# Kernel optimization log

Hardware: AMD Instinct MI355X
Metric: run time of the kernel (lower is better)

The kernel has to match this reference:

```python
import jax, jax.numpy as jnp
import numpy as np

H, NB, D = 16, 64, 1024
HID = 64  # gate MLP hidden width


def setup_inputs() -> dict:
    key = jax.random.key(0)
    ks = jax.random.split(key, 10)
    B, T = 4, 2048
    delta = jax.random.normal(ks[0], (B, T, H, NB), dtype=jnp.float32)
    content_emb = jax.random.normal(ks[1], (B, T, D), dtype=jnp.float32)
    omega = jax.random.normal(ks[2], (H, NB), dtype=jnp.float32)
    # learned parameters
    log_Q = jnp.zeros((H, NB), dtype=jnp.float32)
    log_R = jnp.zeros((H, NB), dtype=jnp.float32)
    log_sigma0 = jnp.full((H, NB), -2.0, dtype=jnp.float32)
    W1 = jax.random.normal(ks[3], (D, HID), dtype=jnp.float32) / np.sqrt(D)
    b1 = jnp.zeros((HID,), dtype=jnp.float32)
    W2 = jax.random.normal(ks[4], (HID, H * NB), dtype=jnp.float32) / np.sqrt(HID)
    b2 = jnp.zeros((H * NB,), dtype=jnp.float32)
    return {"delta": delta, "content_emb": content_emb, "omega": omega,
            "log_Q": log_Q, "log_R": log_R, "log_sigma0": log_sigma0,
            "W1": W1, "b1": b1, "W2": W2, "b2": b2}


def reference(delta, content_emb, omega, log_Q, log_R, log_sigma0, W1, b1, W2, b2):
    B, T, _, _ = delta.shape
    Q = jnp.exp(log_Q)            # (H, NB)
    R = jnp.exp(log_R)            # (H, NB)
    sigma0 = jnp.exp(log_sigma0)  # (H, NB)

    theta_sq = (delta * omega) ** 2  # (B, T, H, NB)

    # landmark gate MLP (exact GELU, as torch default)
    h = jax.nn.gelu(content_emb @ W1 + b1, approximate=False)  # (B, T, HID)
    gates = jax.nn.sigmoid(h @ W2 + b2).reshape(B, T, H, NB)

    def step(sigma, xs):
        theta_sq_t, gate_t = xs  # (B, H, NB) each
        sigma = sigma + Q * theta_sq_t
        K = sigma / (sigma + R)
        sigma = sigma * (1.0 - gate_t * K)
        return sigma, sigma

    init = jnp.broadcast_to(sigma0, (B, H, NB))
    xs = (jnp.swapaxes(theta_sq, 0, 1), jnp.swapaxes(gates, 0, 1))  # (T, B, H, NB)
    _, sigma_seq = jax.lax.scan(step, init, xs)
    sigma = jnp.swapaxes(sigma_seq, 0, 1)  # (B, T, H, NB)
    return sigma, gates
```

## Files before the change

kernel.cpp:

```cpp
#include <hip/hip_runtime.h>
#include <math.h>

#define H_   16
#define NB_  64
#define D_   1024
#define HID_ 64
#define B_   4
#define T_   2048
#define ROWS (B_*T_)
#define HNB  (H_*NB_)

typedef short v8s __attribute__((ext_vector_type(8)));
typedef float v4f __attribute__((ext_vector_type(4)));

__device__ __forceinline__ float gelu_exact(float x) {
    return 0.5f * x * (1.0f + erff(x * 0.7071067811865476f));
}
__device__ __forceinline__ float sigmoidf(float x) {
    return 1.0f / (1.0f + expf(-x));
}
__device__ __forceinline__ ushort f2bf(float x) {
    union { float f; unsigned u; } v; v.f = x;
    unsigned r = v.u + 0x7fffu + ((v.u >> 16) & 1u);
    return (ushort)(r >> 16);
}

__global__ __launch_bounds__(256) void k_prep(const float* __restrict__ W1,
                                              const float* __restrict__ W2,
                                              ushort* __restrict__ w1t,
                                              ushort* __restrict__ w2t) {
    __shared__ float ls[64][65];
    const int t   = threadIdx.x;
    const int blk = blockIdx.x;
    if (blk < 16) {
        const int k0 = blk * 64;
        #pragma unroll
        for (int q = 0; q < 4; ++q) {
            int idx = q * 256 + t;
            int r = idx >> 4, c4 = idx & 15;
            *(float4*)&ls[r][c4 * 4] =
                *(const float4*)&W1[(size_t)(k0 + r) * 64 + c4 * 4];
        }
        __syncthreads();
        const int col = t >> 2, kq = t & 3;
        ushort out[16];
        #pragma unroll
        for (int e = 0; e < 16; ++e) out[e] = f2bf(ls[kq * 16 + e][col]);
        *(uint4*)&w1t[(size_t)col * 1024 + k0 + kq * 16]     = *(uint4*)&out[0];
        *(uint4*)&w1t[(size_t)col * 1024 + k0 + kq * 16 + 8] = *(uint4*)&out[8];
    } else {
        const int n0 = (blk - 16) * 64;
        #pragma unroll
        for (int q = 0; q < 4; ++q) {
            int idx = q * 256 + t;
            int r = idx >> 4, c4 = idx & 15;
            *(float4*)&ls[r][c4 * 4] =
                *(const float4*)&W2[(size_t)r * HNB + n0 + c4 * 4];
        }
        __syncthreads();
        const int n = t >> 2, kq = t & 3;
        ushort out[16];
        #pragma unroll
        for (int e = 0; e < 16; ++e) out[e] = f2bf(ls[kq * 16 + e][n]);
        *(uint4*)&w2t[(size_t)(n0 + n) * 64 + kq * 16]     = *(uint4*)&out[0];
        *(uint4*)&w2t[(size_t)(n0 + n) * 64 + kq * 16 + 8] = *(uint4*)&out[8];
    }
}

__global__ __launch_bounds__(256) void k_gemm1_mfma(const float* __restrict__ X,
                                                    const ushort* __restrict__ w1t,
                                                    const float* __restrict__ b1,
                                                    ushort* __restrict__ hbuf) {
    __shared__ ushort Al[32 * 128];
    __shared__ ushort Bl[64 * 128];
    const int t    = threadIdx.x;
    const int r0   = blockIdx.x * 32;
    const int w    = t >> 6;
    const int lane = t & 63;
    const int lo   = lane & 15;
    const int hi   = lane >> 4;
    const int mt   = w & 1;
    const int nh   = w >> 1;
    const int arow = t >> 3, aseg = t & 7;
    const int brow = t >> 2, bseg = t & 3;

    v4f acc0 = {0.f,0.f,0.f,0.f}, acc1 = {0.f,0.f,0.f,0.f};

    for (int c = 0; c < 8; ++c) {
        float xv[16];
        const float* xp = &X[(size_t)(r0 + arow) * D_ + c * 128 + aseg * 16];
        #pragma unroll
        for (int i = 0; i < 4; ++i) *(float4*)&xv[i*4] = *(const float4*)&xp[i*4];
        ushort wv[32];
        const ushort* wp = &w1t[(size_t)brow * 1024 + c * 128 + bseg * 32];
        #pragma unroll
        for (int i = 0; i < 4; ++i) *(uint4*)&wv[i*8] = *(const uint4*)&wp[i*8];

        __syncthreads();
        #pragma unroll
        for (int j8 = 0; j8 < 2; ++j8) {
            const int k = aseg * 16 + j8 * 8;
            union { ushort u[8]; v8s v; } pa;
            #pragma unroll
            for (int e = 0; e < 8; ++e) pa.u[e] = f2bf(xv[j8 * 8 + e]);
            *(v8s*)&Al[arow * 128 + (k ^ ((arow & 7) << 3))] = pa.v;
        }
        #pragma unroll
        for (int j8 = 0; j8 < 4; ++j8) {
            const int k = bseg * 32 + j8 * 8;
            *(v8s*)&Bl[brow * 128 + (k ^ ((brow & 7) << 3))] = *(v8s*)&wv[j8 * 8];
        }
        __syncthreads();

        const int rowa = mt * 16 + lo;
        #pragma unroll
        for (int kk = 0; kk < 4; ++kk) {
            const int k   = kk * 32 + hi * 8;
            const int sw  = k ^ ((lo & 7) << 3);
            v8s af  = *(v8s*)&Al[rowa * 128 + sw];
            v8s b0  = *(v8s*)&Bl[(nh * 32 + lo) * 128 + sw];
            v8s b1v = *(v8s*)&Bl[(nh * 32 + 16 + lo) * 128 + sw];
            acc0 = __builtin_amdgcn_mfma_f32_16x16x32_bf16(af, b0,  acc0, 0, 0, 0);
            acc1 = __builtin_amdgcn_mfma_f32_16x16x32_bf16(af, b1v, acc1, 0, 0, 0);
        }
    }
    #pragma unroll
    for (int nt = 0; nt < 2; ++nt) {
        v4f a = nt ? acc1 : acc0;
        const int col = nh * 32 + nt * 16 + lo;
        const float bb = b1[col];
        #pragma unroll
        for (int j = 0; j < 4; ++j) {
            const int row = r0 + mt * 16 + hi * 4 + j;
            hbuf[(size_t)row * HID_ + col] = f2bf(gelu_exact(a[j] + bb));
        }
    }
}

__global__ __launch_bounds__(256) void k_gemm2_mfma(const ushort* __restrict__ hbuf,
                                                    const ushort* __restrict__ w2t,
                                                    const float* __restrict__ b2,
                                                    float* __restrict__ gates) {
    __shared__ ushort Ah[64 * 64];
    __shared__ ushort Bh[256 * 64];
    const int t    = threadIdx.x;
    const int r0   = (blockIdx.x >> 2) * 64;
    const int n0   = (blockIdx.x & 3) * 256;
    const int w    = t >> 6;
    const int lane = t & 63;
    const int lo   = lane & 15;
    const int hi   = lane >> 4;

    {
        const int row = t >> 2, seg = t & 3;
        uint4 v0 = *(const uint4*)&hbuf[(size_t)(r0 + row) * 64 + seg * 16];
        uint4 v1 = *(const uint4*)&hbuf[(size_t)(r0 + row) * 64 + seg * 16 + 8];
        const int sw = (row & 7) << 3;
        *(uint4*)&Ah[row * 64 + ((seg * 16) ^ sw)]     = v0;
        *(uint4*)&Ah[row * 64 + ((seg * 16 + 8) ^ sw)] = v1;
    }
    #pragma unroll
    for (int q = 0; q < 4; ++q) {
        const int pi  = q * 256 + t;
        const int n   = pi >> 2, seg = pi & 3;
        uint4 v0 = *(const uint4*)&w2t[(size_t)(n0 + n) * 64 + seg * 16];
        uint4 v1 = *(const uint4*)&w2t[(size_t)(n0 + n) * 64 + seg * 16 + 8];
        const int sw = (n & 7) << 3;
        *(uint4*)&Bh[n * 64 + ((seg * 16) ^ sw)]     = v0;
        *(uint4*)&Bh[n * 64 + ((seg * 16 + 8) ^ sw)] = v1;
    }
    __syncthreads();

    v4f acc[4][4];
    #pragma unroll
    for (int mt = 0; mt < 4; ++mt)
        #pragma unroll
        for (int nt = 0; nt < 4; ++nt) acc[mt][nt] = (v4f){0.f,0.f,0.f,0.f};

    #pragma unroll
    for (int kc = 0; kc < 2; ++kc) {
        const int k  = kc * 32 + hi * 8;
        const int sw = k ^ ((lo & 7) << 3);
        v8s af[4];
        #pragma unroll
        for (int mt = 0; mt < 4; ++mt)
            af[mt] = *(v8s*)&Ah[(mt * 16 + lo) * 64 + sw];
        #pragma unroll
        for (int nt = 0; nt < 4; ++nt) {
            v8s bf = *(v8s*)&Bh[(w * 64 + nt * 16 + lo) * 64 + sw];
            #pragma unroll
            for (int mt = 0; mt < 4; ++mt)
                acc[mt][nt] = __builtin_amdgcn_mfma_f32_16x16x32_bf16(af[mt], bf, acc[mt][nt], 0, 0, 0);
        }
    }

    #pragma unroll
    for (int nt = 0; nt < 4; ++nt) {
        const int col = n0 + w * 64 + nt * 16 + lo;
        const float bb = b2[col];
        #pragma unroll
        for (int mt = 0; mt < 4; ++mt) {
            #pragma unroll
            for (int j = 0; j < 4; ++j) {
                const int row = r0 + mt * 16 + hi * 4 + j;
                gates[(size_t)row * HNB + col] = sigmoidf(acc[mt][nt][j] + bb);
            }
        }
    }
}

#define TT_    32
#define SEGK   8
#define SEGLEN (T_/SEGK)
#define WARMT  3

#define LD8(A, G, grp) { \
    _Pragma("unroll") \
    for (int u = 0; u < 8; ++u) { \
        A[u] = pa[((grp)*8 + u) * 128]; \
        G[u] = pa[((grp)*8 + u) * 128 + 64]; \
    } }

#define CP8(A, G, grp) { \
    _Pragma("unroll") \
    for (int u = 0; u < 8; ++u) { \
        float a   = A[u]; \
        float omg = G[u]; \
        float aR  = a + R; \
        float pc  = fmaf(omg, a, R); \
        float den = sigma + aR; \
        float s   = sigma + a; \
        float pp  = fmaf(omg, sigma, pc); \
        float rc  = __builtin_amdgcn_rcpf(den); \
        float tt  = s * pp; \
        sigma     = tt * rc; \
        ps[((grp)*8 + u) * 64] = sigma; \
    } }

__global__ __launch_bounds__(256) void k_scan_seg(
        const float* __restrict__ delta,
        const float* __restrict__ gates,
        const float* __restrict__ omega,
        const float* __restrict__ log_Q,
        const float* __restrict__ log_R,
        const float* __restrict__ log_s0,
        float* __restrict__ sig) {
    __shared__ float tg_lds[2][TT_][2][64];
    __shared__ float sg_lds[2][TT_][64];
    const int tid = threadIdx.x;
    const int blk = blockIdx.x;
    const int bh  = blk >> 3;
    const int seg = blk & 7;
    const int b   = bh >> 4;
    const int h   = bh & 15;
    const size_t base = (size_t)b * T_ * HNB + h * NB_;
    const int wv   = tid >> 6;
    const int lane = tid & 63;

    const int warm   = (seg == 0) ? 0 : WARMT;
    const int ntiles = SEGLEN / TT_ + warm;
    const int tstart = seg * SEGLEN - warm * TT_;

    float R = 0.f, sigma = 0.f;
    float sc0=0,sc1=0,sc2=0,sc3=0;
    const int col4 = lane & 15;
    const int rg   = lane >> 4;
    const float* dp = delta + base + col4 * 4;
    const float* gp = gates + base + col4 * 4;

    if (wv == 0) {
        const int hn = h * NB_ + lane;
        R     = expf(log_R[hn]);
        sigma = expf(log_s0[hn]);
    } else if (wv == 1) {
        const int hn4 = h * NB_ + col4 * 4;
        float4 om4 = *(const float4*)&omega[hn4];
        float4 lq4 = *(const float4*)&log_Q[hn4];
        sc0 = expf(lq4.x) * om4.x * om4.x;
        sc1 = expf(lq4.y) * om4.y * om4.y;
        sc2 = expf(lq4.z) * om4.z * om4.z;
        sc3 = expf(lq4.w) * om4.w * om4.w;
    }

    for (int p = 0; p <= ntiles + 1; ++p) {
        if (wv == 0) {
            if (p >= 1 && p <= ntiles) {
                const int buf = (p - 1) & 1;
                const float* pa = &tg_lds[buf][0][0][lane];
                float*       ps = &sg_lds[buf][0][lane];
                float a0[8], g0[8], a1[8], g1[8];
                LD8(a0, g0, 0);
                LD8(a1, g1, 1);
                CP8(a0, g0, 0); LD8(a0, g0, 2);
                CP8(a1, g1, 1); LD8(a1, g1, 3);
                CP8(a0, g0, 2);
                CP8(a1, g1, 3);
            }
        } else if (wv == 1) {
            if (p < ntiles) {
                const int buf = p & 1;
                const int t0  = tstart + p * TT_;
                #pragma unroll
                for (int it = 0; it < 8; ++it) {
                    const int row = it * 4 + rg;
                    float4 d = *(const float4*)&dp[(size_t)(t0 + row) * HNB];
                    float4 a;
                    a.x = (sc0 * d.x) * d.x;
                    a.y = (sc1 * d.y) * d.y;
                    a.z = (sc2 * d.z) * d.z;
                    a.w = (sc3 * d.w) * d.w;
                    *(float4*)&tg_lds[buf][row][0][col4 * 4] = a;
                }
            }
        } else if (wv == 2) {
            if (p < ntiles) {
                const int buf = p & 1;
                const int t0  = tstart + p * TT_;
                #pragma unroll
                for (int it = 0; it < 8; ++it) {
                    const int row = it * 4 + rg;
                    float4 g = *(const float4*)&gp[(size_t)(t0 + row) * HNB];
                    float4 o;
                    o.x = 1.0f - g.x; o.y = 1.0f - g.y;
                    o.z = 1.0f - g.z; o.w = 1.0f - g.w;
                    *(float4*)&tg_lds[buf][row][1][col4 * 4] = o;
                }
            }
        } else {
            const int tile = p - 2;
            if (tile >= warm && tile < ntiles) {
                const int buf = p & 1;
                const int t0  = tstart + tile * TT_;
                float* op = sig + base + col4 * 4;
                #pragma unroll
                for (int it = 0; it < 8; ++it) {
                    const int row = it * 4 + rg;
                    float4 v = *(const float4*)&sg_lds[buf][row][col4 * 4];
                    *(float4*)&op[(size_t)(t0 + row) * HNB] = v;
                }
            }
        }
        __syncthreads();
    }
}

extern "C" void kernel_launch(void* const* d_in, const int* in_sizes, int n_in,
                              void* d_out, int out_size, void* d_ws, size_t ws_size,
                              hipStream_t stream) {
    const float* delta   = (const float*)d_in[0];
    const float* content = (const float*)d_in[1];
    const float* omega   = (const float*)d_in[2];
    const float* log_Q   = (const float*)d_in[3];
    const float* log_R   = (const float*)d_in[4];
    const float* log_s0  = (const float*)d_in[5];
    const float* W1      = (const float*)d_in[6];
    const float* b1      = (const float*)d_in[7];
    const float* W2      = (const float*)d_in[8];
    const float* b2      = (const float*)d_in[9];

    float* sig_out   = (float*)d_out;
    float* gates_out = sig_out + (size_t)ROWS * HNB;

    const size_t n_h   = (size_t)ROWS * HID_;
    const size_t n_w1t = (size_t)HID_ * D_;
    const size_t n_w2t = (size_t)HNB * HID_;
    const size_t need  = (n_h + n_w1t + n_w2t) * sizeof(ushort);

    ushort *hbuf, *w1t, *w2t;
    if (ws_size >= need) {
        hbuf = (ushort*)d_ws;
    } else {
        hbuf = (ushort*)sig_out;
    }
    w1t = hbuf + n_h;
    w2t = w1t + n_w1t;

    k_prep<<<32, 256, 0, stream>>>(W1, W2, w1t, w2t);
    k_gemm1_mfma<<<ROWS / 32, 256, 0, stream>>>(content, w1t, b1, hbuf);
    k_gemm2_mfma<<<(ROWS / 64) * 4, 256, 0, stream>>>(hbuf, w2t, b2, gates_out);
    k_scan_seg<<<B_ * H_ * SEGK, 256, 0, stream>>>(delta, gates_out, omega,
                                                   log_Q, log_R, log_s0, sig_out);
}
```

Baseline: 57.42 us.

## Fuse gate GEMM2 and sigmoid into the segmented scan kernel

```diff
diff --git a/kernel.cpp b/kernel.cpp
--- a/kernel.cpp
+++ b/kernel.cpp
@@ -236,6 +236,163 @@
         sigma     = tt * rc; \
         ps[((grp)*8 + u) * 64] = sigma; \
     } }
+
+__global__ __launch_bounds__(256) void k_scan_fused(
+        const float* __restrict__ delta,
+        const ushort* __restrict__ hbuf,
+        const ushort* __restrict__ w2t,
+        const float* __restrict__ b2,
+        const float* __restrict__ omega,
+        const float* __restrict__ log_Q,
+        const float* __restrict__ log_R,
+        const float* __restrict__ log_s0,
+        float* __restrict__ gates,
+        float* __restrict__ sig) {
+    __shared__ float  tg_lds[2][TT_][2][64];
+    __shared__ float  sg_lds[2][TT_][64];
+    __shared__ ushort w2s[64 * 64];
+    const int tid = threadIdx.x;
+    const int blk = blockIdx.x;
+    const int bh  = blk >> 3;
+    const int seg = blk & 7;
+    const int b   = bh >> 4;
+    const int h   = bh & 15;
+    const size_t base = (size_t)b * T_ * HNB + h * NB_;
+    const int wv   = tid >> 6;
+    const int lane = tid & 63;
+    const int lo   = lane & 15;
+    const int hi   = lane >> 4;
+
+    const int warm   = (seg == 0) ? 0 : WARMT;
+    const int ntiles = SEGLEN / TT_ + warm;
+    const int tstart = seg * SEGLEN - warm * TT_;
+
+    float R = 0.f, sigma = 0.f;
+    float sc0=0,sc1=0,sc2=0,sc3=0;
+    float bb0=0,bb1=0,bb2=0,bb3=0;
+    const int col4 = lane & 15;
+    const int rg   = lane >> 4;
+    const float* dp = delta + base + col4 * 4;
+
+    if (wv == 0) {
+        const int hn = h * NB_ + lane;
+        R     = expf(log_R[hn]);
+        sigma = expf(log_s0[hn]);
+    } else if (wv == 1) {
+        const int hn4 = h * NB_ + col4 * 4;
+        float4 om4 = *(const float4*)&omega[hn4];
+        float4 lq4 = *(const float4*)&log_Q[hn4];
+        sc0 = expf(lq4.x) * om4.x * om4.x;
+        sc1 = expf(lq4.y) * om4.y * om4.y;
+        sc2 = expf(lq4.z) * om4.z * om4.z;
+        sc3 = expf(lq4.w) * om4.w * om4.w;
+    } else if (wv == 2) {
+        const ushort* wp = &w2t[(size_t)(h * 64 + lane) * 64];
+        const int sw = (lane & 7) << 3;
+        #pragma unroll
+        for (int s4 = 0; s4 < 4; ++s4) {
+            uint4 v0 = *(const uint4*)&wp[s4 * 16];
+            uint4 v1 = *(const uint4*)&wp[s4 * 16 + 8];
+            *(uint4*)&w2s[lane * 64 + ((s4 * 16) ^ sw)]     = v0;
+            *(uint4*)&w2s[lane * 64 + ((s4 * 16 + 8) ^ sw)] = v1;
+        }
+        bb0 = b2[h * 64 +  0 + lo];
+        bb1 = b2[h * 64 + 16 + lo];
+        bb2 = b2[h * 64 + 32 + lo];
+        bb3 = b2[h * 64 + 48 + lo];
+    }
+
+    for (int p = 0; p <= ntiles + 1; ++p) {
+        if (wv == 0) {
+            if (p >= 1 && p <= ntiles) {
+                const int buf = (p - 1) & 1;
+                const float* pa = &tg_lds[buf][0][0][lane];
+                float*       ps = &sg_lds[buf][0][lane];
+                float a0[8], g0[8], a1[8], g1[8];
+                LD8(a0, g0, 0);
+                LD8(a1, g1, 1);
+                CP8(a0, g0, 0); LD8(a0, g0, 2);
+                CP8(a1, g1, 1); LD8(a1, g1, 3);
+                CP8(a0, g0, 2);
+                CP8(a1, g1, 3);
+            }
+        } else if (wv == 1) {
+            if (p < ntiles) {
+                const int buf = p & 1;
+                const int t0  = tstart + p * TT_;
+                #pragma unroll
+                for (int it = 0; it < 8; ++it) {
+                    const int row = it * 4 + rg;
+                    float4 d = *(const float4*)&dp[(size_t)(t0 + row) * HNB];
+                    float4 a;
+                    a.x = (sc0 * d.x) * d.x;
+                    a.y = (sc1 * d.y) * d.y;
+                    a.z = (sc2 * d.z) * d.z;
+                    a.w = (sc3 * d.w) * d.w;
+                    *(float4*)&tg_lds[buf][row][0][col4 * 4] = a;
+                }
+            }
+        } else if (wv == 2) {
+            if (p < ntiles) {
+                const int buf = p & 1;
+                const int t0  = tstart + p * TT_;
+                const size_t grow = (size_t)b * T_ + t0;
+                v4f acc[2][4];
+                #pragma unroll
+                for (int mt = 0; mt < 2; ++mt)
+                    #pragma unroll
+                    for (int nt = 0; nt < 4; ++nt) acc[mt][nt] = (v4f){0.f,0.f,0.f,0.f};
+                #pragma unroll
+                for (int ks = 0; ks < 2; ++ks) {
+                    const int k  = ks * 32 + hi * 8;
+                    const int sw = k ^ ((lo & 7) << 3);
+                    v8s af[2];
+                    #pragma unroll
+                    for (int mt = 0; mt < 2; ++mt)
+                        af[mt] = *(const v8s*)&hbuf[(grow + mt * 16 + lo) * HID_ + k];
+                    #pragma unroll
+                    for (int nt = 0; nt < 4; ++nt) {
+                        v8s bf = *(v8s*)&w2s[(nt * 16 + lo) * 64 + sw];
+                        #pragma unroll
+                        for (int mt = 0; mt < 2; ++mt)
+                            acc[mt][nt] = __builtin_amdgcn_mfma_f32_16x16x32_bf16(af[mt], bf, acc[mt][nt], 0, 0, 0);
+                    }
+                }
+                const bool wout = (p >= warm);
+                #pragma unroll
+                for (int nt = 0; nt < 4; ++nt) {
+                    const float bb = (nt == 0) ? bb0 : (nt == 1) ? bb1 : (nt == 2) ? bb2 : bb3;
+                    const int col = nt * 16 + lo;
+                    #pragma unroll
+                    for (int mt = 0; mt < 2; ++mt) {
+                        #pragma unroll
+                        for (int j = 0; j < 4; ++j) {
+                            const int row = mt * 16 + hi * 4 + j;
+                            float g = sigmoidf(acc[mt][nt][j] + bb);
+                            tg_lds[buf][row][1][col] = 1.0f - g;
+                            if (wout)
+                                gates[(grow + row) * HNB + h * NB_ + col] = g;
+                        }
+                    }
+                }
+            }
+        } else {
+            const int tile = p - 2;
+            if (tile >= warm && tile < ntiles) {
+                const int buf = p & 1;
+                const int t0  = tstart + tile * TT_;
+                float* op = sig + base + col4 * 4;
+                #pragma unroll
+                for (int it = 0; it < 8; ++it) {
+                    const int row = it * 4 + rg;
+                    float4 v = *(const float4*)&sg_lds[buf][row][col4 * 4];
+                    *(float4*)&op[(size_t)(t0 + row) * HNB] = v;
+                }
+            }
+        }
+        __syncthreads();
+    }
+}
 
 __global__ __launch_bounds__(256) void k_scan_seg(
         const float* __restrict__ delta,
@@ -366,18 +523,23 @@
     const size_t n_w2t = (size_t)HNB * HID_;
     const size_t need  = (n_h + n_w1t + n_w2t) * sizeof(ushort);
 
-    ushort *hbuf, *w1t, *w2t;
     if (ws_size >= need) {
-        hbuf = (ushort*)d_ws;
+        ushort* hbuf = (ushort*)d_ws;
+        ushort* w1t  = hbuf + n_h;
+        ushort* w2t  = w1t + n_w1t;
+        k_prep<<<32, 256, 0, stream>>>(W1, W2, w1t, w2t);
+        k_gemm1_mfma<<<ROWS / 32, 256, 0, stream>>>(content, w1t, b1, hbuf);
+        k_scan_fused<<<B_ * H_ * SEGK, 256, 0, stream>>>(delta, hbuf, w2t, b2,
+                                                         omega, log_Q, log_R,
+                                                         log_s0, gates_out, sig_out);
     } else {
-        hbuf = (ushort*)sig_out;
-    }
-    w1t = hbuf + n_h;
-    w2t = w1t + n_w1t;
-
-    k_prep<<<32, 256, 0, stream>>>(W1, W2, w1t, w2t);
-    k_gemm1_mfma<<<ROWS / 32, 256, 0, stream>>>(content, w1t, b1, hbuf);
-    k_gemm2_mfma<<<(ROWS / 64) * 4, 256, 0, stream>>>(hbuf, w2t, b2, gates_out);
-    k_scan_seg<<<B_ * H_ * SEGK, 256, 0, stream>>>(delta, gates_out, omega,
-                                                   log_Q, log_R, log_s0, sig_out);
-}
+        ushort* hbuf = (ushort*)sig_out;
+        ushort* w1t  = hbuf + n_h;
+        ushort* w2t  = w1t + n_w1t;
+        k_prep<<<32, 256, 0, stream>>>(W1, W2, w1t, w2t);
+        k_gemm1_mfma<<<ROWS / 32, 256, 0, stream>>>(content, w1t, b1, hbuf);
+        k_gemm2_mfma<<<(ROWS / 64) * 4, 256, 0, stream>>>(hbuf, w2t, b2, gates_out);
+        k_scan_seg<<<B_ * H_ * SEGK, 256, 0, stream>>>(delta, gates_out, omega,
+                                                       log_Q, log_R, log_s0, sig_out);
+    }
+}
```

After: 63.88 us. 1.11x slower.

## Fuse gate MLP GEMMs into one kernel keeping hidden activations in LDS

Applied to the files above, without the earlier changes.

```diff
diff --git a/kernel.cpp b/kernel.cpp
--- a/kernel.cpp
+++ b/kernel.cpp
@@ -67,12 +67,16 @@
     }
 }
 
-__global__ __launch_bounds__(256) void k_gemm1_mfma(const float* __restrict__ X,
-                                                    const ushort* __restrict__ w1t,
-                                                    const float* __restrict__ b1,
-                                                    ushort* __restrict__ hbuf) {
+__global__ __launch_bounds__(256) void k_gemm12(const float* __restrict__ X,
+                                                const ushort* __restrict__ w1t,
+                                                const float* __restrict__ b1,
+                                                const ushort* __restrict__ w2t,
+                                                const float* __restrict__ b2,
+                                                float* __restrict__ gates) {
     __shared__ ushort Al[32 * 128];
     __shared__ ushort Bl[64 * 128];
+    __shared__ ushort hs[32 * 64];
+    __shared__ float  gq[4][32][68];
     const int t    = threadIdx.x;
     const int r0   = blockIdx.x * 32;
     const int w    = t >> 6;
@@ -85,7 +89,6 @@
     const int brow = t >> 2, bseg = t & 3;
 
     v4f acc0 = {0.f,0.f,0.f,0.f}, acc1 = {0.f,0.f,0.f,0.f};
-
     for (int c = 0; c < 8; ++c) {
         float xv[16];
         const float* xp = &X[(size_t)(r0 + arow) * D_ + c * 128 + aseg * 16];
@@ -131,81 +134,58 @@
         const float bb = b1[col];
         #pragma unroll
         for (int j = 0; j < 4; ++j) {
-            const int row = r0 + mt * 16 + hi * 4 + j;
-            hbuf[(size_t)row * HID_ + col] = f2bf(gelu_exact(a[j] + bb));
-        }
-    }
-}
-
-__global__ __launch_bounds__(256) void k_gemm2_mfma(const ushort* __restrict__ hbuf,
-                                                    const ushort* __restrict__ w2t,
-                                                    const float* __restrict__ b2,
-                                                    float* __restrict__ gates) {
-    __shared__ ushort Ah[64 * 64];
-    __shared__ ushort Bh[256 * 64];
-    const int t    = threadIdx.x;
-    const int r0   = (blockIdx.x >> 2) * 64;
-    const int n0   = (blockIdx.x & 3) * 256;
-    const int w    = t >> 6;
-    const int lane = t & 63;
-    const int lo   = lane & 15;
-    const int hi   = lane >> 4;
-
-    {
-        const int row = t >> 2, seg = t & 3;
-        uint4 v0 = *(const uint4*)&hbuf[(size_t)(r0 + row) * 64 + seg * 16];
-        uint4 v1 = *(const uint4*)&hbuf[(size_t)(r0 + row) * 64 + seg * 16 + 8];
-        const int sw = (row & 7) << 3;
-        *(uint4*)&Ah[row * 64 + ((seg * 16) ^ sw)]     = v0;
-        *(uint4*)&Ah[row * 64 + ((seg * 16 + 8) ^ sw)] = v1;
-    }
-    #pragma unroll
+            const int row = mt * 16 + hi * 4 + j;
+            hs[row * 64 + (col ^ ((row & 7) << 3))] = f2bf(gelu_exact(a[j] + bb));
+        }
+    }
+    __syncthreads();
+
+    const int n0w = w * 256;
     for (int q = 0; q < 4; ++q) {
-        const int pi  = q * 256 + t;
-        const int n   = pi >> 2, seg = pi & 3;
-        uint4 v0 = *(const uint4*)&w2t[(size_t)(n0 + n) * 64 + seg * 16];
-        uint4 v1 = *(const uint4*)&w2t[(size_t)(n0 + n) * 64 + seg * 16 + 8];
-        const int sw = (n & 7) << 3;
-        *(uint4*)&Bh[n * 64 + ((seg * 16) ^ sw)]     = v0;
-        *(uint4*)&Bh[n * 64 + ((seg * 16 + 8) ^ sw)] = v1;
-    }
-    __syncthreads();
-
-    v4f acc[4][4];
-    #pragma unroll
-    for (int mt = 0; mt < 4; ++mt)
-        #pragma unroll
-        for (int nt = 0; nt < 4; ++nt) acc[mt][nt] = (v4f){0.f,0.f,0.f,0.f};
-
-    #pragma unroll
-    for (int kc = 0; kc < 2; ++kc) {
-        const int k  = kc * 32 + hi * 8;
-        const int sw = k ^ ((lo & 7) << 3);
-        v8s af[4];
-        #pragma unroll
-        for (int mt = 0; mt < 4; ++mt)
-            af[mt] = *(v8s*)&Ah[(mt * 16 + lo) * 64 + sw];
+        v4f acc2[2][4];
+        #pragma unroll
+        for (int m2 = 0; m2 < 2; ++m2)
+            #pragma unroll
+            for (int nt = 0; nt < 4; ++nt) acc2[m2][nt] = (v4f){0.f,0.f,0.f,0.f};
+        #pragma unroll
+        for (int ks = 0; ks < 2; ++ks) {
+            const int k  = ks * 32 + hi * 8;
+            const int sw = k ^ ((lo & 7) << 3);
+            v8s af[2];
+            #pragma unroll
+            for (int m2 = 0; m2 < 2; ++m2)
+                af[m2] = *(v8s*)&hs[(m2 * 16 + lo) * 64 + sw];
+            #pragma unroll
+            for (int nt = 0; nt < 4; ++nt) {
+                const int n = n0w + q * 64 + nt * 16 + lo;
+                v8s bf = *(const v8s*)&w2t[(size_t)n * 64 + k];
+                #pragma unroll
+                for (int m2 = 0; m2 < 2; ++m2)
+                    acc2[m2][nt] = __builtin_amdgcn_mfma_f32_16x16x32_bf16(af[m2], bf, acc2[m2][nt], 0, 0, 0);
+            }
+        }
         #pragma unroll
         for (int nt = 0; nt < 4; ++nt) {
-            v8s bf = *(v8s*)&Bh[(w * 64 + nt * 16 + lo) * 64 + sw];
-            #pragma unroll
-            for (int mt = 0; mt < 4; ++mt)
-                acc[mt][nt] = __builtin_amdgcn_mfma_f32_16x16x32_bf16(af[mt], bf, acc[mt][nt], 0, 0, 0);
-        }
-    }
-
-    #pragma unroll
-    for (int nt = 0; nt < 4; ++nt) {
-        const int col = n0 + w * 64 + nt * 16 + lo;
-        const float bb = b2[col];
-        #pragma unroll
-        for (int mt = 0; mt < 4; ++mt) {
-            #pragma unroll
-            for (int j = 0; j < 4; ++j) {
-                const int row = r0 + mt * 16 + hi * 4 + j;
-                gates[(size_t)row * HNB + col] = sigmoidf(acc[mt][nt][j] + bb);
-            }
-        }
+            const float bb = b2[n0w + q * 64 + nt * 16 + lo];
+            #pragma unroll
+            for (int m2 = 0; m2 < 2; ++m2) {
+                #pragma unroll
+                for (int j = 0; j < 4; ++j) {
+                    const int row = m2 * 16 + hi * 4 + j;
+                    gq[w][row][nt * 16 + lo] = sigmoidf(acc2[m2][nt][j] + bb);
+                }
+            }
+        }
+        __syncthreads();
+        #pragma unroll
+        for (int i = 0; i < 8; ++i) {
+            const int idx = i * 64 + lane;
+            const int row = idx >> 4;
+            const int c4  = idx & 15;
+            float4 v = *(float4*)&gq[w][row][c4 * 4];
+            *(float4*)&gates[(size_t)(r0 + row) * HNB + n0w + q * 64 + c4 * 4] = v;
+        }
+        __syncthreads();
     }
 }
 
@@ -361,23 +341,15 @@
     float* sig_out   = (float*)d_out;
     float* gates_out = sig_out + (size_t)ROWS * HNB;
 
-    const size_t n_h   = (size_t)ROWS * HID_;
     const size_t n_w1t = (size_t)HID_ * D_;
     const size_t n_w2t = (size_t)HNB * HID_;
-    const size_t need  = (n_h + n_w1t + n_w2t) * sizeof(ushort);
-
-    ushort *hbuf, *w1t, *w2t;
-    if (ws_size >= need) {
-        hbuf = (ushort*)d_ws;
-    } else {
-        hbuf = (ushort*)sig_out;
-    }
-    w1t = hbuf + n_h;
-    w2t = w1t + n_w1t;
+    const size_t need  = (n_w1t + n_w2t) * sizeof(ushort);
+
+    ushort* w1t = (ws_size >= need) ? (ushort*)d_ws : (ushort*)sig_out;
+    ushort* w2t = w1t + n_w1t;
 
     k_prep<<<32, 256, 0, stream>>>(W1, W2, w1t, w2t);
-    k_gemm1_mfma<<<ROWS / 32, 256, 0, stream>>>(content, w1t, b1, hbuf);
-    k_gemm2_mfma<<<(ROWS / 64) * 4, 256, 0, stream>>>(hbuf, w2t, b2, gates_out);
+    k_gemm12<<<ROWS / 32, 256, 0, stream>>>(content, w1t, b1, w2t, b2, gates_out);
     k_scan_seg<<<B_ * H_ * SEGK, 256, 0, stream>>>(delta, gates_out, omega,
                                                    log_Q, log_R, log_s0, sig_out);
 }
```

Result: slower. 62.29 us (+8.5%).
